# Kernel tuning notes

Hardware: AMD Instinct MI355X
Metric: run time of the kernel (lower is better)

Reference implementation:

```python
import jax, jax.numpy as jnp
import numpy as np
from jax import lax

FEAT_STRIDE = 16
PRE_NMS_TOPN = 2000
POST_NMS_TOPN = 300
NMS_THRESH = 0.7
MIN_SIZE = 16.0
IMG_H, IMG_W = 1600.0, 2400.0


def _generate_anchors(base_size=16, ratios=(0.5, 1.0, 2.0), scales=(8, 16, 32)):
    w = h = float(base_size)
    xc = yc = 0.5 * (base_size - 1)
    size = w * h
    out = []
    for r in ratios:
        ws = np.round(np.sqrt(size / r))
        hs = np.round(ws * r)
        for s in scales:
            W, H = ws * s, hs * s
            out.append([xc - 0.5 * (W - 1), yc - 0.5 * (H - 1),
                        xc + 0.5 * (W - 1), yc + 0.5 * (H - 1)])
    return np.array(out, dtype=np.float32)  # [9,4]

ANCHORS = jnp.asarray(_generate_anchors())


def _conv(x, w, b, padding):
    y = lax.conv_general_dilated(x, w, (1, 1), padding,
                                 dimension_numbers=('NCHW', 'OIHW', 'NCHW'))
    return y + b[None, :, None, None]


def _nms_mask(boxes, thresh):
    # greedy NMS over score-sorted boxes; returns keep mask
    N = boxes.shape[0]
    x1, y1, x2, y2 = boxes[:, 0], boxes[:, 1], boxes[:, 2], boxes[:, 3]
    areas = (x2 - x1 + 1.0) * (y2 - y1 + 1.0)
    idx = jnp.arange(N)

    def body(i, supp):
        xx1 = jnp.maximum(x1[i], x1)
        yy1 = jnp.maximum(y1[i], y1)
        xx2 = jnp.minimum(x2[i], x2)
        yy2 = jnp.minimum(y2[i], y2)
        w = jnp.maximum(xx2 - xx1 + 1.0, 0.0)
        h = jnp.maximum(yy2 - yy1 + 1.0, 0.0)
        inter = w * h
        iou = inter / (areas[i] + areas - inter)
        cond = (iou > thresh) & (idx > i) & jnp.logical_not(supp[i])
        return supp | cond

    supp = lax.fori_loop(0, N, body, jnp.zeros((N,), dtype=bool))
    return jnp.logical_not(supp)


def reference(features, conv1_w, conv1_b, score_w, score_b, bbox_w, bbox_b, img_info):
    # RPN head
    x = jax.nn.relu(_conv(features, conv1_w, conv1_b, 'SAME'))
    cls = _conv(x, score_w, score_b, 'VALID')    # [1, 2A, H, W]
    deltas = _conv(x, bbox_w, bbox_b, 'VALID')   # [1, 4A, H, W]
    N, C, H, W = cls.shape
    A = C // 2
    # reshape_layer to [N,2,A*H,W], softmax over dim 1, reshape back
    prob = jax.nn.softmax(cls.reshape(N, 2, A * H, W), axis=1).reshape(N, C, H, W)
    fg = prob[:, A:, :, :]                                  # foreground probs
    scores = fg.transpose(0, 2, 3, 1).reshape(-1)           # (H*W*A,)
    d = deltas.transpose(0, 2, 3, 1).reshape(-1, 4)         # (H*W*A, 4)

    # anchor grid (h-major, w-minor, anchor-minor) matching the transpose order
    shift_x = jnp.arange(W, dtype=jnp.float32) * FEAT_STRIDE
    shift_y = jnp.arange(H, dtype=jnp.float32) * FEAT_STRIDE
    sx, sy = jnp.meshgrid(shift_x, shift_y)                 # [H,W]
    shifts = jnp.stack([sx.ravel(), sy.ravel(), sx.ravel(), sy.ravel()], axis=1)
    anchors = (ANCHORS[None, :, :] + shifts[:, None, :]).reshape(-1, 4)

    # bbox_transform_inv decode
    ws = anchors[:, 2] - anchors[:, 0] + 1.0
    hs = anchors[:, 3] - anchors[:, 1] + 1.0
    cx = anchors[:, 0] + 0.5 * ws
    cy = anchors[:, 1] + 0.5 * hs
    pcx = d[:, 0] * ws + cx
    pcy = d[:, 1] * hs + cy
    pw = jnp.exp(d[:, 2]) * ws
    ph = jnp.exp(d[:, 3]) * hs
    props = jnp.stack([pcx - 0.5 * pw, pcy - 0.5 * ph,
                       pcx + 0.5 * pw, pcy + 0.5 * ph], axis=1)
    # clip to image
    props = jnp.stack([jnp.clip(props[:, 0], 0.0, img_info[1] - 1.0),
                       jnp.clip(props[:, 1], 0.0, img_info[0] - 1.0),
                       jnp.clip(props[:, 2], 0.0, img_info[1] - 1.0),
                       jnp.clip(props[:, 3], 0.0, img_info[0] - 1.0)], axis=1)

    # min-size filter (masked, jit-friendly)
    bw = props[:, 2] - props[:, 0] + 1.0
    bh = props[:, 3] - props[:, 1] + 1.0
    min_sz = MIN_SIZE * img_info[2]
    valid = (bw >= min_sz) & (bh >= min_sz)
    scores = jnp.where(valid, scores, -jnp.inf)

    # pre-NMS top-k (sorted desc)
    top_scores, order = lax.top_k(scores, PRE_NMS_TOPN)
    boxes = props[order]
    keep = _nms_mask(boxes, NMS_THRESH)
    kept_scores = jnp.where(keep, top_scores, -jnp.inf)
    post_scores, kidx = lax.top_k(kept_scores, POST_NMS_TOPN)
    final = boxes[kidx]
    rois = jnp.concatenate([jnp.zeros((POST_NMS_TOPN, 1), final.dtype), final], axis=1)
    return rois, post_scores


def setup_inputs() -> dict:
    key = jax.random.key(0)
    ks = jax.random.split(key, 4)
    H, W = 100, 150  # 1600x2400 image at stride 16
    features = jax.random.normal(ks[0], (1, 512, H, W), dtype=jnp.float32)
    conv1_w = jax.random.normal(ks[1], (512, 512, 3, 3), dtype=jnp.float32) * 0.01
    conv1_b = jnp.zeros((512,), dtype=jnp.float32)
    score_w = jax.random.normal(ks[2], (18, 512, 1, 1), dtype=jnp.float32) * 0.01
    score_b = jnp.zeros((18,), dtype=jnp.float32)
    bbox_w = jax.random.normal(ks[3], (36, 512, 1, 1), dtype=jnp.float32) * 0.001
    bbox_b = jnp.zeros((36,), dtype=jnp.float32)
    img_info = jnp.array([IMG_H, IMG_W, 1.0], dtype=jnp.float32)
    return {"features": features, "conv1_w": conv1_w, "conv1_b": conv1_b,
            "score_w": score_w, "score_b": score_b,
            "bbox_w": bbox_w, "bbox_b": bbox_b, "img_info": img_info}
```

## Files before the change

### kernel.cpp

```cpp
#include <hip/hip_runtime.h>
#include <math.h>

#define Hh 100
#define Ww 150
#define Mm 15000
#define NP 135000

typedef double f64x4 __attribute__((ext_vector_type(4)));

#if defined(__HIP_DEVICE_COMPILE__)
#if __has_builtin(__builtin_amdgcn_mfma_f64_16x16x4f64)
#define MFMA64(a,b,c) __builtin_amdgcn_mfma_f64_16x16x4f64((a),(b),(c),0,0,0)
#elif __has_builtin(__builtin_amdgcn_mfma_f64_16x16x4_f64)
#define MFMA64(a,b,c) __builtin_amdgcn_mfma_f64_16x16x4_f64((a),(b),(c),0,0,0)
#else
#error "no f64 mfma builtin on device"
#endif
#else
#define MFMA64(a,b,c) (c)
#endif

__constant__ double ANCH[9][4] = {
  {-84.0,-40.0,99.0,55.0},{-176.0,-88.0,191.0,103.0},{-360.0,-184.0,375.0,191.0},
  {-56.0,-56.0,71.0,71.0},{-120.0,-120.0,135.0,135.0},{-248.0,-248.0,263.0,263.0},
  {-36.0,-80.0,51.0,95.0},{-80.0,-168.0,95.0,183.0},{-168.0,-344.0,183.0,359.0}};

__global__ __launch_bounds__(256) void prep_wT(const float* __restrict__ w,
                                               float* __restrict__ wT) {
  __shared__ float t[32][32][10];
  const int co0 = blockIdx.x * 32, ci0 = blockIdx.y * 32;
  for (int e = threadIdx.x; e < 9216; e += 256) {
    int cr = e / 288;
    int rem = e - cr * 288;
    int cir = rem / 9, tap = rem - cir * 9;
    t[cir][cr][tap] = w[(size_t)(co0 + cr) * 4608 + (ci0 + cir) * 9 + tap];
  }
  __syncthreads();
  for (int e = threadIdx.x; e < 9216; e += 256) {
    int tap = e / 1024;
    int rem = e - tap * 1024;
    int cir = rem >> 5, cr = rem & 31;
    wT[(size_t)tap * 262144 + (size_t)(ci0 + cir) * 512 + (co0 + cr)] = t[cir][cr][tap];
  }
}

__global__ void prep_w54(const float* __restrict__ sw, const float* __restrict__ bw,
                         double* __restrict__ w54) {
  int idx = blockIdx.x * 256 + threadIdx.x;
  if (idx < 54 * 512) {
    int o = idx >> 9, c = idx & 511;
    w54[idx] = (double)((o < 18) ? sw[o * 512 + c] : bw[(o - 18) * 512 + c]);
  }
}

__global__ __launch_bounds__(256, 2) void conv3x3(const float* __restrict__ feat,
                                                  const float* __restrict__ wT,
                                                  const float* __restrict__ bias,
                                                  float* __restrict__ x) {
  __shared__ union {
    struct { float A[32][72]; float B[32][136]; } s;
    float Lx[128][65];
  } sm;
  const int tid = threadIdx.x;
  const int lane = tid & 63;
  const int wv = tid >> 6;
  const int pw = (wv & 1) * 32;
  const int cw = (wv >> 1) * 64;
  const int m0 = blockIdx.x * 64;
  const int n0 = blockIdx.y * 128;
  const int l15 = lane & 15, l4 = lane >> 4;

  f64x4 zero; zero[0] = 0.0; zero[1] = 0.0; zero[2] = 0.0; zero[3] = 0.0;
  const double ap1 = (l4 == 0) ? (double)l15 : 0.0;
  const double bp1 = (l4 == 0) ? 1.0 : 0.0;
  const f64x4 rowp = MFMA64(ap1, bp1, zero);
  const double ap2 = (l4 == 0) ? 1.0 : 0.0;
  const double bp2 = (l4 == 0) ? (double)l15 : 0.0;
  const f64x4 colp = MFMA64(ap2, bp2, zero);
  int rowm[4], colm[4];
#pragma unroll
  for (int r = 0; r < 4; ++r) { rowm[r] = (int)rowp[r]; colm[r] = (int)colp[r]; }

  f64x4 acc[2][4];
#pragma unroll
  for (int i = 0; i < 2; ++i)
#pragma unroll
    for (int q = 0; q < 4; ++q) acc[i][q] = zero;

  const int pa = tid & 63;
  const int ka = (tid >> 6) * 8;
  const int ma = m0 + pa;
  const int ha = ma / 150, wa = ma - ha * 150;
  const int cq = tid & 31;
  const int kb = (tid >> 5) * 4;

  for (int tap = 0; tap < 9; ++tap) {
    const int dy = tap / 3 - 1, dx = tap % 3 - 1;
    const int hh = ha + dy, wwp = wa + dx;
    const bool ok = (ma < Mm) && (hh >= 0) && (hh < Hh) && (wwp >= 0) && (wwp < Ww);
    const int src = hh * Ww + wwp;
    const float* wb = wT + (size_t)tap * 262144 + n0;
    for (int cb = 0; cb < 512; cb += 32) {
#pragma unroll
      for (int kk = 0; kk < 8; ++kk)
        sm.s.A[ka + kk][pa] = ok ? feat[(size_t)(cb + ka + kk) * Mm + src] : 0.0f;
#pragma unroll
      for (int kk = 0; kk < 4; ++kk)
        *(float4*)&sm.s.B[kb + kk][cq * 4] = *(const float4*)&wb[(size_t)(cb + kb + kk) * 512 + cq * 4];
      __syncthreads();
#pragma unroll
      for (int t = 0; t < 8; ++t) {
        const int kt = t * 4 + l4;
        const double a0 = (double)sm.s.A[kt][pw + l15];
        const double a1 = (double)sm.s.A[kt][pw + 16 + l15];
        const double b0 = (double)sm.s.B[kt][cw + l15];
        const double b1 = (double)sm.s.B[kt][cw + 16 + l15];
        const double b2 = (double)sm.s.B[kt][cw + 32 + l15];
        const double b3 = (double)sm.s.B[kt][cw + 48 + l15];
        acc[0][0] = MFMA64(a0, b0, acc[0][0]);
        acc[0][1] = MFMA64(a0, b1, acc[0][1]);
        acc[0][2] = MFMA64(a0, b2, acc[0][2]);
        acc[0][3] = MFMA64(a0, b3, acc[0][3]);
        acc[1][0] = MFMA64(a1, b0, acc[1][0]);
        acc[1][1] = MFMA64(a1, b1, acc[1][1]);
        acc[1][2] = MFMA64(a1, b2, acc[1][2]);
        acc[1][3] = MFMA64(a1, b3, acc[1][3]);
      }
      __syncthreads();
    }
  }
#pragma unroll
  for (int i = 0; i < 2; ++i)
#pragma unroll
    for (int q = 0; q < 4; ++q)
#pragma unroll
      for (int r = 0; r < 4; ++r) {
        const int row = pw + i * 16 + rowm[r];
        const int col = cw + q * 16 + colm[r];
        const double v = acc[i][q][r] + (double)bias[n0 + col];
        sm.Lx[col][row] = (float)(v > 0.0 ? v : 0.0);
      }
  __syncthreads();
  for (int e = tid; e < 64 * 128; e += 256) {
    const int co = e >> 6, p = e & 63;
    const int m = m0 + p;
    if (m < Mm) x[(size_t)(n0 + co) * Mm + m] = sm.Lx[co][p];
  }
}

__global__ __launch_bounds__(256) void conv1x1(const float* __restrict__ x,
                                               const double* __restrict__ w54,
                                               const float* __restrict__ sb,
                                               const float* __restrict__ bb,
                                               float* __restrict__ cls,
                                               float* __restrict__ dl) {
  int m = blockIdx.x * 256 + threadIdx.x;
  int g = blockIdx.y;
  double acc[9];
#pragma unroll
  for (int o = 0; o < 9; ++o) acc[o] = 0.0;
  if (m < Mm) {
    const double* wg = w54 + (size_t)g * 9 * 512;
    for (int c = 0; c < 512; ++c) {
      double v = (double)x[(size_t)c * Mm + m];
#pragma unroll
      for (int o = 0; o < 9; ++o) acc[o] += v * wg[o * 512 + c];
    }
#pragma unroll
    for (int o = 0; o < 9; ++o) {
      int oo = g * 9 + o;
      if (oo < 18) cls[oo * Mm + m] = (float)(acc[o] + (double)sb[oo]);
      else dl[(oo - 18) * Mm + m] = (float)(acc[o] + (double)bb[oo - 18]);
    }
  }
}

__global__ void decode(const float* __restrict__ cls, const float* __restrict__ dl,
                       const float* __restrict__ info, double4* __restrict__ props,
                       float* __restrict__ scoresF, unsigned long long* __restrict__ keys64,
                       unsigned* __restrict__ keys32) {
  int i = blockIdx.x * 256 + threadIdx.x;
  if (i >= NP) return;
  int m = i / 9, a = i - m * 9;
  int h = m / 150, w = m - h * 150;
  double c0 = (double)cls[a * Mm + m], c1 = (double)cls[(9 + a) * Mm + m];
  double mx = fmax(c0, c1);
  double e0 = exp(c0 - mx), e1 = exp(c1 - mx);
  double p = e1 / (e0 + e1);
  double d0 = (double)dl[(a * 4 + 0) * Mm + m], d1 = (double)dl[(a * 4 + 1) * Mm + m];
  double d2 = (double)dl[(a * 4 + 2) * Mm + m], d3 = (double)dl[(a * 4 + 3) * Mm + m];
  double sx = (double)w * 16.0, sy = (double)h * 16.0;
  double ax1 = ANCH[a][0] + sx, ay1 = ANCH[a][1] + sy;
  double ax2 = ANCH[a][2] + sx, ay2 = ANCH[a][3] + sy;
  double aw = ax2 - ax1 + 1.0, ah = ay2 - ay1 + 1.0;
  double cx = ax1 + 0.5 * aw, cy = ay1 + 0.5 * ah;
  double pcx = d0 * aw + cx, pcy = d1 * ah + cy;
  double pw = exp(d2) * aw, ph = exp(d3) * ah;
  double x1 = pcx - 0.5 * pw, y1 = pcy - 0.5 * ph;
  double x2 = pcx + 0.5 * pw, y2 = pcy + 0.5 * ph;
  double IH = (double)info[0], IW = (double)info[1], sc = (double)info[2];
  x1 = fmin(fmax(x1, 0.0), IW - 1.0); y1 = fmin(fmax(y1, 0.0), IH - 1.0);
  x2 = fmin(fmax(x2, 0.0), IW - 1.0); y2 = fmin(fmax(y2, 0.0), IH - 1.0);
  double bwd = x2 - x1 + 1.0, bhd = y2 - y1 + 1.0;
  bool valid = (bwd >= 16.0 * sc) && (bhd >= 16.0 * sc);
  double score = valid ? p : -__builtin_inf();
  double4 pr; pr.x = x1; pr.y = y1; pr.z = x2; pr.w = y2;
  props[i] = pr;
  float pf = (float)score;
  scoresF[i] = pf;
  unsigned long long b = (unsigned long long)__double_as_longlong(score);
  unsigned long long s = (b >> 63) ? ~b : (b | 0x8000000000000000ull);
  unsigned long long k = ~s;
  keys64[i] = (k & ~0x3FFFFull) | (unsigned long long)i;
  unsigned ub = __float_as_uint(pf);
  unsigned us = (ub >> 31) ? ~ub : (ub | 0x80000000u);
  keys32[i] = ~us;
}

__global__ void hist_k(const unsigned* __restrict__ keys32, unsigned* __restrict__ hist) {
  int i = blockIdx.x * 256 + threadIdx.x;
  if (i < NP) atomicAdd(&hist[keys32[i] >> 16], 1u);
}

__global__ __launch_bounds__(1024) void cutoff_k(const unsigned* __restrict__ hist,
                                                 int* __restrict__ Bout) {
  __shared__ unsigned ps[1024];
  int t = threadIdx.x;
  unsigned s = 0;
  for (int b = t * 64; b < t * 64 + 64; ++b) s += hist[b];
  ps[t] = s; __syncthreads();
  for (int off = 1; off < 1024; off <<= 1) {
    unsigned a = ps[t];
    unsigned bb2 = (t >= off) ? ps[t - off] : 0u;
    __syncthreads();
    ps[t] = a + bb2;
    __syncthreads();
  }
  unsigned excl = ps[t] - s;
  if (excl < 2000u) {
    unsigned run = excl;
    for (int b = t * 64; b < t * 64 + 64; ++b) {
      unsigned nb = run + hist[b];
      if (run < 2000u && nb >= 2000u) *Bout = b;
      run = nb;
    }
  }
}

__global__ void compact_k(const unsigned* __restrict__ keys32,
                          const unsigned long long* __restrict__ keys64,
                          const int* __restrict__ Bptr,
                          unsigned long long* __restrict__ cand, int* __restrict__ cnt) {
  int i = blockIdx.x * 256 + threadIdx.x;
  if (i >= NP) return;
  int B = *Bptr;
  if ((int)(keys32[i] >> 16) <= B) {
    int pos = atomicAdd(cnt, 1);
    if (pos < 8192) cand[pos] = keys64[i];
  }
}

__global__ __launch_bounds__(1024) void sort_top(const unsigned long long* __restrict__ cand,
                                                 const int* __restrict__ pcnt,
                                                 const double4* __restrict__ props,
                                                 const float* __restrict__ scoresF,
                                                 double4* __restrict__ boxes2000,
                                                 float* __restrict__ score2000) {
  __shared__ unsigned long long sh[8192];
  int t = threadIdx.x;
  int cnt = *pcnt; if (cnt > 8192) cnt = 8192;
  for (int i = t; i < 8192; i += 1024) sh[i] = (i < cnt) ? cand[i] : ~0ull;
  __syncthreads();
  for (int kb = 1; kb <= 13; ++kb) {
    int k = 1 << kb;
    for (int jb = kb - 1; jb >= 0; --jb) {
      int j = 1 << jb;
      for (int s = t; s < 4096; s += 1024) {
        int i = ((s >> jb) << (jb + 1)) | (s & (j - 1));
        int l = i + j;
        bool up = ((i & k) == 0);
        unsigned long long a = sh[i], b = sh[l];
        if (up ? (a > b) : (a < b)) { sh[i] = b; sh[l] = a; }
      }
      __syncthreads();
    }
  }
  for (int r = t; r < 2000; r += 1024) {
    unsigned long long key = sh[r];
    int idx = (int)(key & 0x3FFFFull);
    boxes2000[r] = props[idx];
    score2000[r] = scoresF[idx];
  }
}

__global__ __launch_bounds__(256) void nms_mask(const double4* __restrict__ boxes,
                                                unsigned long long* __restrict__ mask) {
  int tid = threadIdx.x;
  int r = blockIdx.x * 8 + (tid >> 5);
  int wd = tid & 31;
  double4 bi = boxes[r];
  double ai = (bi.z - bi.x + 1.0) * (bi.w - bi.y + 1.0);
  unsigned long long bits = 0;
  int j0 = wd * 64;
  int jmax = 2000 - j0; if (jmax > 64) jmax = 64;
  for (int jj = 0; jj < jmax; ++jj) {
    int j = j0 + jj;
    if (j > r) {
      double4 bj = boxes[j];
      double xx1 = fmax(bi.x, bj.x), yy1 = fmax(bi.y, bj.y);
      double xx2 = fmin(bi.z, bj.z), yy2 = fmin(bi.w, bj.w);
      double w_ = fmax(xx2 - xx1 + 1.0, 0.0), h_ = fmax(yy2 - yy1 + 1.0, 0.0);
      double inter = w_ * h_;
      double aj = (bj.z - bj.x + 1.0) * (bj.w - bj.y + 1.0);
      double iou = inter / (ai + aj - inter);
      if (iou > 0.7) bits |= 1ull << jj;
    }
  }
  mask[r * 32 + wd] = bits;
}

__global__ __launch_bounds__(256) void suppress(const unsigned long long* __restrict__ mask,
                                                unsigned long long* __restrict__ aliveOut) {
  __shared__ unsigned long long rows[64][32];
  int tid = threadIdx.x;
  int lane = tid & 63;
  unsigned long long myword = 0;
  if (tid < 64) {
    if (lane < 31) myword = ~0ull;
    else if (lane == 31) myword = 0xFFFFull;
  }
  for (int c = 0; c < 32; ++c) {
    __syncthreads();
    for (int idx = tid; idx < 2048; idx += 256) {
      int g = c * 2048 + idx;
      ((unsigned long long*)rows)[idx] = (g < 64000) ? mask[g] : 0ull;
    }
    __syncthreads();
    if (tid < 64) {
      for (int r = 0; r < 64; ++r) {
        int i = c * 64 + r;
        unsigned long long rw = rows[r][lane & 31];
        unsigned long long aw = __shfl(myword, i >> 6);
        if ((aw >> (i & 63)) & 1ull) {
          if (lane < 32) myword &= ~rw;
        }
      }
    }
  }
  __syncthreads();
  if (tid < 32) aliveOut[tid] = myword;
}

__global__ __launch_bounds__(1024) void finalize(const unsigned long long* __restrict__ alive,
                                                 const double4* __restrict__ boxes,
                                                 const float* __restrict__ scores,
                                                 float* __restrict__ out) {
  __shared__ int ps[1024];
  int t = threadIdx.x;
  int e0 = 2 * t, e1 = 2 * t + 1;
  int f0 = (e0 < 2000) ? (int)((alive[e0 >> 6] >> (e0 & 63)) & 1ull) : 0;
  int f1 = (e1 < 2000) ? (int)((alive[e1 >> 6] >> (e1 & 63)) & 1ull) : 0;
  int v = f0 + f1;
  ps[t] = v; __syncthreads();
  for (int off = 1; off < 1024; off <<= 1) {
    int a = ps[t];
    int b = (t >= off) ? ps[t - off] : 0;
    __syncthreads();
    ps[t] = a + b;
    __syncthreads();
  }
  int incl = ps[t];
  int excl = incl - v;
  int Na = ps[1023];
  if (f0 && excl < 300) {
    double4 bx = boxes[e0];
    out[excl * 5 + 0] = 0.f; out[excl * 5 + 1] = (float)bx.x; out[excl * 5 + 2] = (float)bx.y;
    out[excl * 5 + 3] = (float)bx.z; out[excl * 5 + 4] = (float)bx.w;
    out[1500 + excl] = scores[e0];
  }
  int p1 = excl + f0;
  if (f1 && p1 < 300) {
    double4 bx = boxes[e1];
    out[p1 * 5 + 0] = 0.f; out[p1 * 5 + 1] = (float)bx.x; out[p1 * 5 + 2] = (float)bx.y;
    out[p1 * 5 + 3] = (float)bx.z; out[p1 * 5 + 4] = (float)bx.w;
    out[1500 + p1] = scores[e1];
  }
  if (Na < 300) {
    if (e0 < 2000 && !f0) {
      int q = Na + (e0 - excl);
      if (q < 300) {
        double4 bx = boxes[e0];
        out[q * 5 + 0] = 0.f; out[q * 5 + 1] = (float)bx.x; out[q * 5 + 2] = (float)bx.y;
        out[q * 5 + 3] = (float)bx.z; out[q * 5 + 4] = (float)bx.w;
        out[1500 + q] = -__builtin_inff();
      }
    }
    if (e1 < 2000 && !f1) {
      int q = Na + (e1 - (excl + f0));
      if (q < 300) {
        double4 bx = boxes[e1];
        out[q * 5 + 0] = 0.f; out[q * 5 + 1] = (float)bx.x; out[q * 5 + 2] = (float)bx.y;
        out[q * 5 + 3] = (float)bx.z; out[q * 5 + 4] = (float)bx.w;
        out[1500 + q] = -__builtin_inff();
      }
    }
  }
}

extern "C" void kernel_launch(void* const* d_in, const int* in_sizes, int n_in,
                              void* d_out, int out_size, void* d_ws, size_t ws_size,
                              hipStream_t stream) {
  (void)in_sizes; (void)n_in; (void)out_size; (void)ws_size;
  const float* feat = (const float*)d_in[0];
  const float* w1   = (const float*)d_in[1];
  const float* b1   = (const float*)d_in[2];
  const float* sw   = (const float*)d_in[3];
  const float* sb   = (const float*)d_in[4];
  const float* bw   = (const float*)d_in[5];
  const float* bb   = (const float*)d_in[6];
  const float* info = (const float*)d_in[7];
  float* out = (float*)d_out;

  char* ws = (char*)d_ws;
  size_t off = 0;
  auto alloc = [&](size_t bytes) -> void* {
    void* p = ws + off;
    off += (bytes + 255) & ~(size_t)255;
    return p;
  };
  float* x        = (float*)alloc((size_t)512 * Mm * 4);
  float* wT       = (float*)alloc((size_t)9 * 512 * 512 * 4);
  double* w54     = (double*)alloc((size_t)54 * 512 * 8);
  float* cls      = (float*)alloc((size_t)18 * Mm * 4);
  float* dl       = (float*)alloc((size_t)36 * Mm * 4);
  double4* props  = (double4*)alloc((size_t)NP * 32);
  float* scoresF  = (float*)alloc((size_t)NP * 4);
  unsigned long long* keys64 = (unsigned long long*)alloc((size_t)NP * 8);
  unsigned* keys32 = (unsigned*)alloc((size_t)NP * 4);
  unsigned* hist   = (unsigned*)alloc((size_t)65536 * 4);
  int* Bptr        = (int*)alloc(256);
  int* cnt         = (int*)alloc(256);
  unsigned long long* cand = (unsigned long long*)alloc((size_t)8192 * 8);
  double4* boxes2000 = (double4*)alloc((size_t)2000 * 32);
  float* score2000   = (float*)alloc((size_t)2000 * 4);
  unsigned long long* mask  = (unsigned long long*)alloc((size_t)2000 * 32 * 8);
  unsigned long long* alive = (unsigned long long*)alloc((size_t)32 * 8);

  hipMemsetAsync(hist, 0, 65536 * 4, stream);
  hipMemsetAsync(cnt, 0, 4, stream);

  prep_wT<<<dim3(16, 16), 256, 0, stream>>>(w1, wT);
  prep_w54<<<108, 256, 0, stream>>>(sw, bw, w54);
  conv3x3<<<dim3(235, 4), 256, 0, stream>>>(feat, wT, b1, x);
  conv1x1<<<dim3(59, 6), 256, 0, stream>>>(x, w54, sb, bb, cls, dl);
  decode<<<528, 256, 0, stream>>>(cls, dl, info, props, scoresF, keys64, keys32);
  hist_k<<<528, 256, 0, stream>>>(keys32, hist);
  cutoff_k<<<1, 1024, 0, stream>>>(hist, Bptr);
  compact_k<<<528, 256, 0, stream>>>(keys32, keys64, Bptr, cand, cnt);
  sort_top<<<1, 1024, 0, stream>>>(cand, cnt, props, scoresF, boxes2000, score2000);
  nms_mask<<<250, 256, 0, stream>>>(boxes2000, mask);
  suppress<<<1, 256, 0, stream>>>(mask, alive);
  finalize<<<1, 1024, 0, stream>>>(alive, boxes2000, score2000, out);
}
```

Measured before the change: 1.960 ms.

## Double-buffer conv3x3 LDS tiles with register prefetch and fuse histogram into decode

The conv3x3 main loop is flattened over 144 tap/channel chunks. Global loads for chunk c+2 now go into registers while chunk c is computed from one of two LDS buffers, so only one barrier is needed per chunk instead of two. The launch bound is raised to three blocks per CU, and the histogram atomicAdd moves into the decode kernel, which removes a separate launch and a reread of keys32. In exchange the kernel uses more LDS and prefetch registers, and the tighter occupancy bound may cause register spills.

```diff
diff --git a/kernel.cpp b/kernel.cpp
--- a/kernel.cpp
+++ b/kernel.cpp
@@ -53,12 +53,12 @@
   }
 }
 
-__global__ __launch_bounds__(256, 2) void conv3x3(const float* __restrict__ feat,
+__global__ __launch_bounds__(256, 3) void conv3x3(const float* __restrict__ feat,
                                                   const float* __restrict__ wT,
                                                   const float* __restrict__ bias,
                                                   float* __restrict__ x) {
   __shared__ union {
-    struct { float A[32][72]; float B[32][136]; } s;
+    struct { float A[2][32][72]; float B[2][32][136]; } s;
     float Lx[128][65];
   } sm;
   const int tid = threadIdx.x;
@@ -94,41 +94,63 @@
   const int cq = tid & 31;
   const int kb = (tid >> 5) * 4;
 
-  for (int tap = 0; tap < 9; ++tap) {
-    const int dy = tap / 3 - 1, dx = tap % 3 - 1;
+  float aR[8];
+  float4 bR[4];
+
+  auto loadRegs = [&](int c) {
+    const int tap = c >> 4;
+    const int cb = (c & 15) << 5;
+    const int dy = tap / 3 - 1, dx = tap - (tap / 3) * 3 - 1;
     const int hh = ha + dy, wwp = wa + dx;
     const bool ok = (ma < Mm) && (hh >= 0) && (hh < Hh) && (wwp >= 0) && (wwp < Ww);
     const int src = hh * Ww + wwp;
+#pragma unroll
+    for (int kk = 0; kk < 8; ++kk)
+      aR[kk] = ok ? feat[(size_t)(cb + ka + kk) * Mm + src] : 0.0f;
     const float* wb = wT + (size_t)tap * 262144 + n0;
-    for (int cb = 0; cb < 512; cb += 32) {
-#pragma unroll
-      for (int kk = 0; kk < 8; ++kk)
-        sm.s.A[ka + kk][pa] = ok ? feat[(size_t)(cb + ka + kk) * Mm + src] : 0.0f;
-#pragma unroll
-      for (int kk = 0; kk < 4; ++kk)
-        *(float4*)&sm.s.B[kb + kk][cq * 4] = *(const float4*)&wb[(size_t)(cb + kb + kk) * 512 + cq * 4];
+#pragma unroll
+    for (int kk = 0; kk < 4; ++kk)
+      bR[kk] = *(const float4*)&wb[(size_t)(cb + kb + kk) * 512 + cq * 4];
+  };
+  auto writeLDS = [&](int b) {
+#pragma unroll
+    for (int kk = 0; kk < 8; ++kk) sm.s.A[b][ka + kk][pa] = aR[kk];
+#pragma unroll
+    for (int kk = 0; kk < 4; ++kk) *(float4*)&sm.s.B[b][kb + kk][cq * 4] = bR[kk];
+  };
+
+  loadRegs(0);
+  writeLDS(0);
+  loadRegs(1);
+  __syncthreads();
+
+  for (int c = 0; c < 144; ++c) {
+    const int b = c & 1;
+#pragma unroll
+    for (int t = 0; t < 8; ++t) {
+      const int kt = t * 4 + l4;
+      const double a0 = (double)sm.s.A[b][kt][pw + l15];
+      const double a1 = (double)sm.s.A[b][kt][pw + 16 + l15];
+      const double b0 = (double)sm.s.B[b][kt][cw + l15];
+      const double b1 = (double)sm.s.B[b][kt][cw + 16 + l15];
+      const double b2 = (double)sm.s.B[b][kt][cw + 32 + l15];
+      const double b3 = (double)sm.s.B[b][kt][cw + 48 + l15];
+      acc[0][0] = MFMA64(a0, b0, acc[0][0]);
+      acc[0][1] = MFMA64(a0, b1, acc[0][1]);
+      acc[0][2] = MFMA64(a0, b2, acc[0][2]);
+      acc[0][3] = MFMA64(a0, b3, acc[0][3]);
+      acc[1][0] = MFMA64(a1, b0, acc[1][0]);
+      acc[1][1] = MFMA64(a1, b1, acc[1][1]);
+      acc[1][2] = MFMA64(a1, b2, acc[1][2]);
+      acc[1][3] = MFMA64(a1, b3, acc[1][3]);
+    }
+    if (c + 1 < 144) {
+      writeLDS(b ^ 1);
+      if (c + 2 < 144) loadRegs(c + 2);
       __syncthreads();
-#pragma unroll
-      for (int t = 0; t < 8; ++t) {
-        const int kt = t * 4 + l4;
-        const double a0 = (double)sm.s.A[kt][pw + l15];
-        const double a1 = (double)sm.s.A[kt][pw + 16 + l15];
-        const double b0 = (double)sm.s.B[kt][cw + l15];
-        const double b1 = (double)sm.s.B[kt][cw + 16 + l15];
-        const double b2 = (double)sm.s.B[kt][cw + 32 + l15];
-        const double b3 = (double)sm.s.B[kt][cw + 48 + l15];
-        acc[0][0] = MFMA64(a0, b0, acc[0][0]);
-        acc[0][1] = MFMA64(a0, b1, acc[0][1]);
-        acc[0][2] = MFMA64(a0, b2, acc[0][2]);
-        acc[0][3] = MFMA64(a0, b3, acc[0][3]);
-        acc[1][0] = MFMA64(a1, b0, acc[1][0]);
-        acc[1][1] = MFMA64(a1, b1, acc[1][1]);
-        acc[1][2] = MFMA64(a1, b2, acc[1][2]);
-        acc[1][3] = MFMA64(a1, b3, acc[1][3]);
-      }
-      __syncthreads();
-    }
-  }
+    }
+  }
+  __syncthreads();
 #pragma unroll
   for (int i = 0; i < 2; ++i)
 #pragma unroll
@@ -178,7 +200,7 @@
 __global__ void decode(const float* __restrict__ cls, const float* __restrict__ dl,
                        const float* __restrict__ info, double4* __restrict__ props,
                        float* __restrict__ scoresF, unsigned long long* __restrict__ keys64,
-                       unsigned* __restrict__ keys32) {
+                       unsigned* __restrict__ keys32, unsigned* __restrict__ hist) {
   int i = blockIdx.x * 256 + threadIdx.x;
   if (i >= NP) return;
   int m = i / 9, a = i - m * 9;
@@ -214,12 +236,9 @@
   keys64[i] = (k & ~0x3FFFFull) | (unsigned long long)i;
   unsigned ub = __float_as_uint(pf);
   unsigned us = (ub >> 31) ? ~ub : (ub | 0x80000000u);
-  keys32[i] = ~us;
-}
-
-__global__ void hist_k(const unsigned* __restrict__ keys32, unsigned* __restrict__ hist) {
-  int i = blockIdx.x * 256 + threadIdx.x;
-  if (i < NP) atomicAdd(&hist[keys32[i] >> 16], 1u);
+  unsigned k32 = ~us;
+  keys32[i] = k32;
+  atomicAdd(&hist[k32 >> 16], 1u);
 }
 
 __global__ __launch_bounds__(1024) void cutoff_k(const unsigned* __restrict__ hist,
@@ -453,8 +472,7 @@
   prep_w54<<<108, 256, 0, stream>>>(sw, bw, w54);
   conv3x3<<<dim3(235, 4), 256, 0, stream>>>(feat, wT, b1, x);
   conv1x1<<<dim3(59, 6), 256, 0, stream>>>(x, w54, sb, bb, cls, dl);
-  decode<<<528, 256, 0, stream>>>(cls, dl, info, props, scoresF, keys64, keys32);
-  hist_k<<<528, 256, 0, stream>>>(keys32, hist);
+  decode<<<528, 256, 0, stream>>>(cls, dl, info, props, scoresF, keys64, keys32, hist);
   cutoff_k<<<1, 1024, 0, stream>>>(hist, Bptr);
   compact_k<<<528, 256, 0, stream>>>(keys32, keys64, Bptr, cand, cnt);
   sort_top<<<1, 1024, 0, stream>>>(cand, cnt, props, scoresF, boxes2000, score2000);
```

Result: slower. 2.001 ms (+2.1%).
